# Performance work log

Measured on AMD Instinct MI355X. Metric: run time of the kernel, lower is better.

## Reference

```python
import jax, jax.numpy as jnp
import numpy as np

BETA = 0.25


def setup_inputs() -> dict:
    key = jax.random.key(0)
    k1, k2 = jax.random.split(key)
    x = jax.random.normal(k1, (32, 64, 64, 64), dtype=jnp.float32)   # [B, C, H, W]
    emb = jax.random.normal(k2, (1024, 64), dtype=jnp.float32)       # [K, C] codebook
    return {"x": x, "emb": emb}


def reference(x, emb):
    b, c, h, w = x.shape
    # (b h w) c
    z = jnp.transpose(x, (0, 2, 3, 1)).reshape(-1, c)
    # squared euclidean distances (argmin identical to torch.cdist argmin)
    # ||z||^2 - 2 z e^T + ||e||^2, never taking sqrt since only argmin is used
    d = (jnp.sum(z * z, axis=1, keepdims=True)
         - 2.0 * jnp.einsum('nc,kc->nk', z, emb)
         + jnp.sum(emb * emb, axis=1)[None, :])        # [N, K]
    idx = jnp.argmin(d, axis=1)                        # [N] int
    e = emb[idx]                                       # gather [N, C]
    e = jnp.transpose(e.reshape(b, h, w, c), (0, 3, 1, 2))  # [B, C, H, W]
    codebook_loss = jnp.mean((jax.lax.stop_gradient(x) - e) ** 2)
    commitment_loss = BETA * jnp.mean((x - jax.lax.stop_gradient(e)) ** 2)
    loss = codebook_loss + commitment_loss
    o = x + jax.lax.stop_gradient(e - x)               # straight-through
    indices = idx.reshape(b, h, w)
    return (o, loss, indices)
```

## Files before the change

kernel.cpp:

```cpp
#include <hip/hip_runtime.h>

#define BATCH   32
#define CCH     64
#define HW      4096
#define NPIX    (BATCH * HW)
#define KCODES  1024
#define NELEM   (NPIX * CCH)
#define MB      256
#define CK      64
#define MARGIN_Q 3u

typedef _Float16 f16;
typedef __attribute__((ext_vector_type(8))) _Float16 f16x8;
typedef __attribute__((ext_vector_type(4))) float    f32x4;

static __device__ __forceinline__ f32x4 mfma16(f16x8 a, f16x8 b, f32x4 c) {
    return __builtin_amdgcn_mfma_f32_16x16x32_f16(a, b, c, 0, 0, 0);
}

static __device__ __forceinline__ void dma16(void* lds, const void* g) {
    __builtin_amdgcn_global_load_lds(
        (const __attribute__((address_space(1))) unsigned int*)g,
        (__attribute__((address_space(3))) unsigned int*)lds, 16, 0, 0);
}

#define WS_EEB_F   64
#define WS_CBH_B   8192
#define WS_CBL_B   139264
#define WS_WL_U    67584

__global__ __launch_bounds__(256) void vq_prep(
    const float* __restrict__ emb, float* __restrict__ wsf,
    unsigned* __restrict__ wsu, f16* __restrict__ cbH, f16* __restrict__ cbL,
    float* __restrict__ eeb_g)
{
    const int t = threadIdx.x;
    if (blockIdx.x < 32) {
        const int gid = blockIdx.x * 256 + t;
        const int row = gid >> 3, gi = gid & 7;
        const float* src = emb + (size_t)row * CCH + gi * 8;
        float4 v0 = *(const float4*)(src);
        float4 v1 = *(const float4*)(src + 4);
        float vv[8] = {v0.x, v0.y, v0.z, v0.w, v1.x, v1.y, v1.z, v1.w};
        f16x8 h, l;
#pragma unroll
        for (int j = 0; j < 8; ++j) {
            f16 hh = (f16)vv[j];
            h[j] = hh;
            l[j] = (f16)(vv[j] - (float)hh);
        }
        const int off = row * 64 + 8 * (gi ^ (row & 7));
        *(f16x8*)(cbH + off) = h;
        *(f16x8*)(cbL + off) = l;
    } else {
        if (t == 0) { wsf[0] = 0.f; wsu[1] = 0u; }
        for (int r = t * 4; r < t * 4 + 4; ++r) {
            const float4* row4 = (const float4*)(emb + (size_t)r * CCH);
            float s = 0.f;
#pragma unroll
            for (int i = 0; i < 16; ++i) {
                float4 v = row4[i];
                s = fmaf(v.x, v.x, s); s = fmaf(v.y, v.y, s);
                s = fmaf(v.z, v.z, s); s = fmaf(v.w, v.w, s);
            }
            eeb_g[r] = fmaf(s, 2048.0f, 1048576.0f);
        }
    }
}

__global__ __launch_bounds__(256, 2) void vq_main(
    const float* __restrict__ x,
    const float* __restrict__ emb,
    const f16* __restrict__ cbH, const f16* __restrict__ cbL,
    const float* __restrict__ eeb_g,
    float* __restrict__ o, float* __restrict__ idx_out,
    float* __restrict__ acc, unsigned* __restrict__ wl_count,
    unsigned* __restrict__ wl, unsigned cap)
{
    __shared__ __align__(16) char smem[32768];
    __shared__ float eebl[2][CK];
    __shared__ unsigned bu1[MB], bu2[MB];
    __shared__ float wred[4];

    const int t    = threadIdx.x;
    const int lane = t & 63;
    const int w    = t >> 6;
    const int col  = lane & 15;
    const int quad = lane >> 4;
    const int c7   = col & 7;
    const int sw0  = 8 * (quad ^ c7);
    const int sw1  = sw0 ^ 32;
    const int n0   = blockIdx.x * MB;
    const int b    = n0 >> 12;
    const int p0   = n0 & 4095;
    const float* xb = x + (size_t)b * (CCH * HW) + p0;

    auto stage = [&](int chunk, int bufi) {
        const int k0 = chunk * CK;
        char* lb = smem + bufi * 16384;
        const char* gH = (const char*)cbH + (size_t)k0 * 128 + w * 2048 + lane * 16;
        const char* gL = (const char*)cbL + (size_t)k0 * 128 + w * 2048 + lane * 16;
        char* lH = lb + w * 2048;
        char* lL = lb + 8192 + w * 2048;
        dma16(lH,        gH);
        dma16(lH + 1024, gH + 1024);
        dma16(lL,        gL);
        dma16(lL + 1024, gL + 1024);
        if (t < CK) eebl[bufi][t] = eeb_g[k0 + t];
    };

    stage(0, 0);

    f16x8 aH[4][2], aL[4][2];
#pragma unroll
    for (int rt = 0; rt < 4; ++rt) {
        const int pp = w * 64 + rt * 16 + col;
#pragma unroll
        for (int kc = 0; kc < 2; ++kc) {
            f16x8 h, l;
#pragma unroll
            for (int j = 0; j < 8; ++j) {
                const int c = kc * 32 + quad * 8 + j;
                float zs = -2.0f * xb[(size_t)c * HW + pp];
                f16 hh = (f16)zs;
                h[j] = hh;
                l[j] = (f16)(zs - (float)hh);
            }
            aH[rt][kc] = h;
            aL[rt][kc] = l;
        }
    }

    unsigned best[16], best2[16];
#pragma unroll
    for (int s = 0; s < 16; ++s) { best[s] = 0xFFFFFFFFu; best2[s] = 0xFFFFFFFFu; }

    for (int chunk = 0; chunk < KCODES / CK; ++chunk) {
        const int cur = chunk & 1;
        __syncthreads();
        if (chunk + 1 < KCODES / CK) stage(chunk + 1, cur ^ 1);

        const f16* bufH = (const f16*)(smem + cur * 16384);
        const f16* bufL = bufH + 4096;
        const int k0 = chunk * CK;

#pragma unroll
        for (int tile = 0; tile < CK / 16; ++tile) {
            const f16* bh = bufH + (tile * 16 + col) * 64;
            const f16* bl = bufL + (tile * 16 + col) * 64;
            f16x8 bH0 = *(const f16x8*)(bh + sw0);
            f16x8 bH1 = *(const f16x8*)(bh + sw1);
            f16x8 bL0 = *(const f16x8*)(bl + sw0);
            f16x8 bL1 = *(const f16x8*)(bl + sw1);
            const float eebc = eebl[cur][tile * 16 + col];
            const unsigned kb = (unsigned)(k0 + tile * 16 + col);
#pragma unroll
            for (int rt = 0; rt < 4; ++rt) {
                f32x4 a4 = {0.f, 0.f, 0.f, 0.f};
                a4 = mfma16(aH[rt][0], bH0, a4);
                a4 = mfma16(aH[rt][1], bH1, a4);
                a4 = mfma16(aL[rt][0], bH0, a4);
                a4 = mfma16(aL[rt][1], bH1, a4);
                a4 = mfma16(aH[rt][0], bL0, a4);
                a4 = mfma16(aH[rt][1], bL1, a4);
#pragma unroll
                for (int r = 0; r < 4; ++r) {
                    float uf = fmaf(a4[r], 2048.0f, eebc);
                    unsigned pk = (((unsigned)uf) << 10) | kb;
                    const int s = rt * 4 + r;
                    best2[s] = min(best2[s], max(pk, best[s]));
                    best[s]  = min(best[s], pk);
                }
            }
        }
    }

#pragma unroll
    for (int d = 1; d < 16; d <<= 1) {
#pragma unroll
        for (int s = 0; s < 16; ++s) {
            unsigned ob  = __shfl_xor(best[s],  d, 64);
            unsigned ob2 = __shfl_xor(best2[s], d, 64);
            best2[s] = min(min(best2[s], ob2), max(best[s], ob));
            best[s]  = min(best[s], ob);
        }
    }
    if (col == 0) {
#pragma unroll
        for (int rt = 0; rt < 4; ++rt)
#pragma unroll
            for (int r = 0; r < 4; ++r) {
                const int pl = w * 64 + rt * 16 + quad * 4 + r;
                bu1[pl] = best[rt * 4 + r];
                bu2[pl] = best2[rt * 4 + r];
            }
    }
    __syncthreads();

    const unsigned bu = bu1[t];
    const unsigned bidx = bu & 1023u;
    idx_out[n0 + t] = (float)bidx;
    {
        const unsigned qg = (bu2[t] >> 10) - (bu >> 10);
        if (qg < MARGIN_Q) {
            unsigned pos = atomicAdd(wl_count, 1u);
            if (pos < cap) wl[pos] = (unsigned)(n0 + t);
        }
    }
    float ss = 0.f;
    {
        const float4* er4 = (const float4*)(emb + (size_t)bidx * CCH);
        const float* xbt = xb + t;
        float* ob = o + (size_t)b * (CCH * HW) + p0 + t;
#pragma unroll
        for (int i = 0; i < 16; ++i) {
            float4 ev = er4[i];
            float evv[4] = {ev.x, ev.y, ev.z, ev.w};
#pragma unroll
            for (int q = 0; q < 4; ++q) {
                const int c = i * 4 + q;
                float xv = xbt[(size_t)c * HW];
                float e  = evv[q];
                ob[(size_t)c * HW] = xv + (e - xv);
                float d = xv - e;
                ss = fmaf(d, d, ss);
            }
        }
    }
    for (int off = 32; off; off >>= 1) ss += __shfl_down(ss, off, 64);
    if (lane == 0) wred[w] = ss;
    __syncthreads();
    if (t == 0) atomicAdd(acc, (wred[0] + wred[1]) + (wred[2] + wred[3]));
}

__global__ __launch_bounds__(256) void vq_refine(
    const float* __restrict__ x, const float* __restrict__ emb,
    float* __restrict__ o, float* __restrict__ idx_out,
    float* __restrict__ acc, const unsigned* __restrict__ wl_count,
    const unsigned* __restrict__ wl, unsigned cap)
{
    __shared__ float zsh[CCH];
    __shared__ double rbd[4];
    __shared__ int rbi[4];
    __shared__ int s_pk;
    unsigned cnt = *wl_count; if (cnt > cap) cnt = cap;
    const int t = threadIdx.x;

    for (unsigned i = blockIdx.x; i < cnt; i += gridDim.x) {
        const int n = (int)wl[i];
        const int b = n >> 12, p = n & 4095;
        if (t < CCH) zsh[t] = x[(size_t)b * (CCH * HW) + (size_t)t * HW + p];
        __syncthreads();

        double bd = 1e300; int bi = KCODES;
        for (int j = 0; j < 4; ++j) {
            const int k = t + j * 256;
            const float* er = emb + (size_t)k * CCH;
            double d = 0.0;
#pragma unroll
            for (int c = 0; c < CCH; ++c) {
                double tt = (double)zsh[c] - (double)er[c];
                d = fma(tt, tt, d);
            }
            if (d < bd) { bd = d; bi = k; }
        }
        for (int dlt = 1; dlt < 64; dlt <<= 1) {
            double od = __shfl_xor(bd, dlt, 64);
            int    oi = __shfl_xor(bi, dlt, 64);
            if (od < bd || (od == bd && oi < bi)) { bd = od; bi = oi; }
        }
        const int wv = t >> 6;
        if ((t & 63) == 0) { rbd[wv] = bd; rbi[wv] = bi; }
        __syncthreads();
        if (t == 0) {
            double fb = rbd[0]; int fi = rbi[0];
            for (int q = 1; q < 4; ++q)
                if (rbd[q] < fb || (rbd[q] == fb && rbi[q] < fi)) { fb = rbd[q]; fi = rbi[q]; }
            const int old = (int)idx_out[n];
            if (fi != old) { idx_out[n] = (float)fi; s_pk = (old << 16) | fi; }
            else s_pk = -1;
        }
        __syncthreads();
        const int pk = s_pk;
        if (pk >= 0 && t < CCH) {
            const int old = pk >> 16, fi = pk & 0xFFFF;
            const float xv = zsh[t];
            const float eo = emb[(size_t)old * CCH + t];
            const float en = emb[(size_t)fi  * CCH + t];
            o[(size_t)b * (CCH * HW) + (size_t)t * HW + p] = xv + (en - xv);
            const float dn = xv - en, dd = xv - eo;
            float delta = dn * dn - dd * dd;
            for (int off = 32; off; off >>= 1) delta += __shfl_down(delta, off, 64);
            if (t == 0) atomicAdd(acc, delta);
        }
        __syncthreads();
    }
}

__global__ void vq_fin(const float* __restrict__ acc, float* __restrict__ loss) {
    *loss = 1.25f * (*acc) * (1.0f / (float)NELEM);
}

extern "C" void kernel_launch(void* const* d_in, const int* in_sizes, int n_in,
                              void* d_out, int out_size, void* d_ws, size_t ws_size,
                              hipStream_t stream) {
    const float* x   = (const float*)d_in[0];
    const float* emb = (const float*)d_in[1];
    float*    out = (float*)d_out;
    float*    wsf = (float*)d_ws;
    unsigned* wsu = (unsigned*)d_ws;
    char*     wsb = (char*)d_ws;

    float* o_out    = out;
    float* loss_out = out + NELEM;
    float* idx_out  = out + NELEM + 1;
    float* eeb_g    = wsf + WS_EEB_F;
    f16*   cbH      = (f16*)(wsb + WS_CBH_B);
    f16*   cbL      = (f16*)(wsb + WS_CBL_B);
    unsigned* wl    = wsu + WS_WL_U;
    unsigned cap = 0;
    if (ws_size / 4 > WS_WL_U) {
        size_t c = ws_size / 4 - WS_WL_U;
        cap = (unsigned)(c > NPIX ? NPIX : c);
    }

    vq_prep<<<33, 256, 0, stream>>>(emb, wsf, wsu, cbH, cbL, eeb_g);
    vq_main<<<NPIX / MB, 256, 0, stream>>>(x, emb, cbH, cbL, eeb_g, o_out,
                                           idx_out, wsf, wsu + 1, wl, cap);
    vq_refine<<<512, 256, 0, stream>>>(x, emb, o_out, idx_out, wsf,
                                       wsu + 1, wl, cap);
    vq_fin<<<1, 1, 0, stream>>>(wsf, loss_out);
}
```

Baseline: 159.8 us.

## Use 512-thread main blocks, fuse loss finalize into refine, merge prep

The main kernel now runs 8 waves per 256-pixel block, with each wave handling 32 pixels instead of 64. This halves per-thread accumulator and A-fragment registers and raises occupancy through launch bounds of (512,4). The top-2 tracking uses v_med3_u32. The prep kernel computes codebook norms with a shuffle reduction inside the same blocks that split the codebook, dropping the extra block. The final loss kernel is folded into refine through a last-block-done counter, which removes one launch but adds an atomic handshake.

Measured after the change: 175.6 us. +9.9%, slower.

```diff
diff --git a/kernel.cpp b/kernel.cpp
--- a/kernel.cpp
+++ b/kernel.cpp
@@ -24,6 +24,12 @@
         (__attribute__((address_space(3))) unsigned int*)lds, 16, 0, 0);
 }
 
+static __device__ __forceinline__ unsigned med3u(unsigned a, unsigned b, unsigned c) {
+    unsigned d;
+    asm("v_med3_u32 %0, %1, %2, %3" : "=v"(d) : "v"(a), "v"(b), "v"(c));
+    return d;
+}
+
 #define WS_EEB_F   64
 #define WS_CBH_B   8192
 #define WS_CBL_B   139264
@@ -34,41 +40,33 @@
     unsigned* __restrict__ wsu, f16* __restrict__ cbH, f16* __restrict__ cbL,
     float* __restrict__ eeb_g)
 {
-    const int t = threadIdx.x;
-    if (blockIdx.x < 32) {
-        const int gid = blockIdx.x * 256 + t;
-        const int row = gid >> 3, gi = gid & 7;
-        const float* src = emb + (size_t)row * CCH + gi * 8;
-        float4 v0 = *(const float4*)(src);
-        float4 v1 = *(const float4*)(src + 4);
-        float vv[8] = {v0.x, v0.y, v0.z, v0.w, v1.x, v1.y, v1.z, v1.w};
-        f16x8 h, l;
-#pragma unroll
-        for (int j = 0; j < 8; ++j) {
-            f16 hh = (f16)vv[j];
-            h[j] = hh;
-            l[j] = (f16)(vv[j] - (float)hh);
-        }
-        const int off = row * 64 + 8 * (gi ^ (row & 7));
-        *(f16x8*)(cbH + off) = h;
-        *(f16x8*)(cbL + off) = l;
-    } else {
-        if (t == 0) { wsf[0] = 0.f; wsu[1] = 0u; }
-        for (int r = t * 4; r < t * 4 + 4; ++r) {
-            const float4* row4 = (const float4*)(emb + (size_t)r * CCH);
-            float s = 0.f;
-#pragma unroll
-            for (int i = 0; i < 16; ++i) {
-                float4 v = row4[i];
-                s = fmaf(v.x, v.x, s); s = fmaf(v.y, v.y, s);
-                s = fmaf(v.z, v.z, s); s = fmaf(v.w, v.w, s);
-            }
-            eeb_g[r] = fmaf(s, 2048.0f, 1048576.0f);
-        }
-    }
-}
-
-__global__ __launch_bounds__(256, 2) void vq_main(
+    const int t   = threadIdx.x;
+    const int gid = blockIdx.x * 256 + t;
+    const int row = gid >> 3, gi = gid & 7;
+    if (gid == 0) { wsf[0] = 0.f; wsu[1] = 0u; wsu[2] = 0u; }
+    const float* src = emb + (size_t)row * CCH + gi * 8;
+    float4 v0 = *(const float4*)(src);
+    float4 v1 = *(const float4*)(src + 4);
+    float vv[8] = {v0.x, v0.y, v0.z, v0.w, v1.x, v1.y, v1.z, v1.w};
+    f16x8 h, l;
+    float s = 0.f;
+#pragma unroll
+    for (int j = 0; j < 8; ++j) {
+        f16 hh = (f16)vv[j];
+        h[j] = hh;
+        l[j] = (f16)(vv[j] - (float)hh);
+        s = fmaf(vv[j], vv[j], s);
+    }
+    const int off = row * 64 + 8 * (gi ^ (row & 7));
+    *(f16x8*)(cbH + off) = h;
+    *(f16x8*)(cbL + off) = l;
+    s += __shfl_xor(s, 1, 64);
+    s += __shfl_xor(s, 2, 64);
+    s += __shfl_xor(s, 4, 64);
+    if (gi == 0) eeb_g[row] = fmaf(s, 2048.0f, 1048576.0f);
+}
+
+__global__ __launch_bounds__(512, 4) void vq_main(
     const float* __restrict__ x,
     const float* __restrict__ emb,
     const f16* __restrict__ cbH, const f16* __restrict__ cbL,
@@ -80,7 +78,7 @@
     __shared__ __align__(16) char smem[32768];
     __shared__ float eebl[2][CK];
     __shared__ unsigned bu1[MB], bu2[MB];
-    __shared__ float wred[4];
+    __shared__ float wred[8];
 
     const int t    = threadIdx.x;
     const int lane = t & 63;
@@ -98,23 +96,19 @@
     auto stage = [&](int chunk, int bufi) {
         const int k0 = chunk * CK;
         char* lb = smem + bufi * 16384;
-        const char* gH = (const char*)cbH + (size_t)k0 * 128 + w * 2048 + lane * 16;
-        const char* gL = (const char*)cbL + (size_t)k0 * 128 + w * 2048 + lane * 16;
-        char* lH = lb + w * 2048;
-        char* lL = lb + 8192 + w * 2048;
-        dma16(lH,        gH);
-        dma16(lH + 1024, gH + 1024);
-        dma16(lL,        gL);
-        dma16(lL + 1024, gL + 1024);
+        const char* gH = (const char*)cbH + (size_t)k0 * 128 + w * 1024 + lane * 16;
+        const char* gL = (const char*)cbL + (size_t)k0 * 128 + w * 1024 + lane * 16;
+        dma16(lb + w * 1024,        gH);
+        dma16(lb + 8192 + w * 1024, gL);
         if (t < CK) eebl[bufi][t] = eeb_g[k0 + t];
     };
 
     stage(0, 0);
 
-    f16x8 aH[4][2], aL[4][2];
-#pragma unroll
-    for (int rt = 0; rt < 4; ++rt) {
-        const int pp = w * 64 + rt * 16 + col;
+    f16x8 aH[2][2], aL[2][2];
+#pragma unroll
+    for (int rt = 0; rt < 2; ++rt) {
+        const int pp = w * 32 + rt * 16 + col;
 #pragma unroll
         for (int kc = 0; kc < 2; ++kc) {
             f16x8 h, l;
@@ -131,9 +125,11 @@
         }
     }
 
-    unsigned best[16], best2[16];
-#pragma unroll
-    for (int s = 0; s < 16; ++s) { best[s] = 0xFFFFFFFFu; best2[s] = 0xFFFFFFFFu; }
+    unsigned best[8], best2[8];
+#pragma unroll
+    for (int s = 0; s < 8; ++s) { best[s] = 0xFFFFFFFFu; best2[s] = 0xFFFFFFFFu; }
+
+    const f32x4 zero4 = {0.f, 0.f, 0.f, 0.f};
 
     for (int chunk = 0; chunk < KCODES / CK; ++chunk) {
         const int cur = chunk & 1;
@@ -155,9 +151,8 @@
             const float eebc = eebl[cur][tile * 16 + col];
             const unsigned kb = (unsigned)(k0 + tile * 16 + col);
 #pragma unroll
-            for (int rt = 0; rt < 4; ++rt) {
-                f32x4 a4 = {0.f, 0.f, 0.f, 0.f};
-                a4 = mfma16(aH[rt][0], bH0, a4);
+            for (int rt = 0; rt < 2; ++rt) {
+                f32x4 a4 = mfma16(aH[rt][0], bH0, zero4);
                 a4 = mfma16(aH[rt][1], bH1, a4);
                 a4 = mfma16(aL[rt][0], bH0, a4);
                 a4 = mfma16(aL[rt][1], bH1, a4);
@@ -168,8 +163,9 @@
                     float uf = fmaf(a4[r], 2048.0f, eebc);
                     unsigned pk = (((unsigned)uf) << 10) | kb;
                     const int s = rt * 4 + r;
-                    best2[s] = min(best2[s], max(pk, best[s]));
-                    best[s]  = min(best[s], pk);
+                    const unsigned b0 = best[s];
+                    best2[s] = med3u(b0, best2[s], pk);
+                    best[s]  = min(b0, pk);
                 }
             }
         }
@@ -178,7 +174,7 @@
 #pragma unroll
     for (int d = 1; d < 16; d <<= 1) {
 #pragma unroll
-        for (int s = 0; s < 16; ++s) {
+        for (int s = 0; s < 8; ++s) {
             unsigned ob  = __shfl_xor(best[s],  d, 64);
             unsigned ob2 = __shfl_xor(best2[s], d, 64);
             best2[s] = min(min(best2[s], ob2), max(best[s], ob));
@@ -187,21 +183,23 @@
     }
     if (col == 0) {
 #pragma unroll
-        for (int rt = 0; rt < 4; ++rt)
+        for (int rt = 0; rt < 2; ++rt)
 #pragma unroll
             for (int r = 0; r < 4; ++r) {
-                const int pl = w * 64 + rt * 16 + quad * 4 + r;
+                const int pl = w * 32 + rt * 16 + quad * 4 + r;
                 bu1[pl] = best[rt * 4 + r];
                 bu2[pl] = best2[rt * 4 + r];
             }
     }
     __syncthreads();
 
-    const unsigned bu = bu1[t];
+    const int pix  = t & 255;
+    const int half = t >> 8;
+    const unsigned bu = bu1[pix];
     const unsigned bidx = bu & 1023u;
-    idx_out[n0 + t] = (float)bidx;
-    {
-        const unsigned qg = (bu2[t] >> 10) - (bu >> 10);
+    if (half == 0) {
+        idx_out[n0 + t] = (float)bidx;
+        const unsigned qg = (bu2[pix] >> 10) - (bu >> 10);
         if (qg < MARGIN_Q) {
             unsigned pos = atomicAdd(wl_count, 1u);
             if (pos < cap) wl[pos] = (unsigned)(n0 + t);
@@ -209,16 +207,16 @@
     }
     float ss = 0.f;
     {
-        const float4* er4 = (const float4*)(emb + (size_t)bidx * CCH);
-        const float* xbt = xb + t;
-        float* ob = o + (size_t)b * (CCH * HW) + p0 + t;
-#pragma unroll
-        for (int i = 0; i < 16; ++i) {
+        const float4* er4 = (const float4*)(emb + (size_t)bidx * CCH) + half * 8;
+        const float* xbt = xb + pix;
+        float* ob = o + (size_t)b * (CCH * HW) + p0 + pix;
+#pragma unroll
+        for (int i = 0; i < 8; ++i) {
             float4 ev = er4[i];
             float evv[4] = {ev.x, ev.y, ev.z, ev.w};
 #pragma unroll
             for (int q = 0; q < 4; ++q) {
-                const int c = i * 4 + q;
+                const int c = half * 32 + i * 4 + q;
                 float xv = xbt[(size_t)c * HW];
                 float e  = evv[q];
                 ob[(size_t)c * HW] = xv + (e - xv);
@@ -230,14 +228,20 @@
     for (int off = 32; off; off >>= 1) ss += __shfl_down(ss, off, 64);
     if (lane == 0) wred[w] = ss;
     __syncthreads();
-    if (t == 0) atomicAdd(acc, (wred[0] + wred[1]) + (wred[2] + wred[3]));
+    if (t == 0) {
+        float s2 = 0.f;
+#pragma unroll
+        for (int q = 0; q < 8; ++q) s2 += wred[q];
+        atomicAdd(acc, s2);
+    }
 }
 
 __global__ __launch_bounds__(256) void vq_refine(
     const float* __restrict__ x, const float* __restrict__ emb,
     float* __restrict__ o, float* __restrict__ idx_out,
     float* __restrict__ acc, const unsigned* __restrict__ wl_count,
-    const unsigned* __restrict__ wl, unsigned cap)
+    const unsigned* __restrict__ wl, unsigned cap,
+    float* __restrict__ loss, unsigned* __restrict__ done)
 {
     __shared__ float zsh[CCH];
     __shared__ double rbd[4];
@@ -295,10 +299,16 @@
         }
         __syncthreads();
     }
-}
-
-__global__ void vq_fin(const float* __restrict__ acc, float* __restrict__ loss) {
-    *loss = 1.25f * (*acc) * (1.0f / (float)NELEM);
+
+    __threadfence();
+    if (t == 0) {
+        unsigned prev = atomicAdd(done, 1u);
+        if (prev + 1 == gridDim.x) {
+            __threadfence();
+            float a = atomicAdd(acc, 0.0f);
+            loss[0] = 1.25f * a * (1.0f / (float)NELEM);
+        }
+    }
 }
 
 extern "C" void kernel_launch(void* const* d_in, const int* in_sizes, int n_in,
@@ -324,10 +334,9 @@
         cap = (unsigned)(c > NPIX ? NPIX : c);
     }
 
-    vq_prep<<<33, 256, 0, stream>>>(emb, wsf, wsu, cbH, cbL, eeb_g);
-    vq_main<<<NPIX / MB, 256, 0, stream>>>(x, emb, cbH, cbL, eeb_g, o_out,
+    vq_prep<<<32, 256, 0, stream>>>(emb, wsf, wsu, cbH, cbL, eeb_g);
+    vq_main<<<NPIX / MB, 512, 0, stream>>>(x, emb, cbH, cbL, eeb_g, o_out,
                                            idx_out, wsf, wsu + 1, wl, cap);
     vq_refine<<<512, 256, 0, stream>>>(x, emb, o_out, idx_out, wsf,
-                                       wsu + 1, wl, cap);
-    vq_fin<<<1, 1, 0, stream>>>(wsf, loss_out);
-}
+                                       wsu + 1, wl, cap, loss_out, wsu + 2);
+}
```
